# Kernel optimization log

Measured on AMD Instinct MI355X. Metric: run time of the kernel, lower is better.

## Reference

```python
import jax, jax.numpy as jnp
import numpy as np

# Model constants (from init_kwargs)
D, P, M_STEPS, H = 32, 8, 50, 128
INTERVAL, SIGMA = 1.0, 1.0
N = 32768


def setup_inputs() -> dict:
    key = jax.random.key(0)
    ks = jax.random.split(key, 7)
    return {
        "observations": jax.random.normal(ks[0], (P,), jnp.float32),
        "initial_states": jax.random.normal(ks[1], (N, D), jnp.float32),
        "initial_values": jax.random.normal(ks[2], (N,), jnp.float32),
        "noise": jax.random.normal(ks[3], (M_STEPS, N, D), jnp.float32),
        "W1": jax.random.normal(ks[4], (D + P + 2, H), jnp.float32) * 0.05,
        "b1": jnp.zeros((H,), jnp.float32),
        "W2": jax.random.normal(ks[5], (H, D), jnp.float32) * 0.05,
        "b2": jnp.zeros((D,), jnp.float32),
        "theta": jax.random.uniform(ks[6], (1,), jnp.float32, 0.1, 1.0),
        "obs_index": 3,
        "control_required": 1,
    }


def reference(observations, initial_states, initial_values, noise,
              W1, b1, W2, b2, theta, obs_index, control_required):
    dt = jnp.float32(INTERVAL / M_STEPS)
    sqrt_dt = jnp.sqrt(dt)
    times = jnp.linspace(0.0, INTERVAL, M_STEPS + 1, dtype=jnp.float32)[:M_STEPS]
    n = initial_states.shape[0]
    Yb = jnp.broadcast_to(observations, (n, P))          # (N, p)
    t_feat = jnp.full((n, 1), float(obs_index), jnp.float32)
    cr = jnp.float32(control_required)

    def z_net(s, X):
        # Z_Network: MLP over [X, Y, s, t] -> (N, d)
        feats = jnp.concatenate([X, Yb, jnp.full((n, 1), s, jnp.float32), t_feat], axis=1)
        h = jnp.tanh(feats @ W1 + b1)
        return h @ W2 + b2

    def step(carry, xs):
        X, V = carry
        noise_m, s = xs
        W = sqrt_dt * noise_m                            # Brownian increment (N, d)
        Z = z_net(s, X)                                  # (N, d)
        control = -jax.lax.stop_gradient(Z) * cr         # detach + flag
        drift_V = 0.5 * jnp.sum(jnp.square(Z), axis=1) + jnp.sum(control * Z, axis=1)
        V = V + dt * drift_V + jnp.sum(Z * W, axis=1)
        drift_X = -theta * X + SIGMA * control           # b(theta, X) = -theta * X (OU drift)
        X = X + dt * drift_X + SIGMA * W
        return (X, V), None

    (X, V), _ = jax.lax.scan(step, (initial_states, initial_values), (noise, times))
    return X, V
```

## Files before the change

kernel.cpp:

```cpp
#include <hip/hip_runtime.h>
#include <math.h>

#define NPART 32768
#define MS 50
#define BLOCK 256

typedef __attribute__((ext_vector_type(8))) short bfrag;
typedef __attribute__((ext_vector_type(4))) float ffrag;

__device__ __forceinline__ unsigned short f2bf(float x) {
    unsigned u = __float_as_uint(x);
    u += 0x7fffu + ((u >> 16) & 1u);
    return (unsigned short)(u >> 16);
}

#if __has_builtin(__builtin_amdgcn_cvt_pk_bf16_f32)
typedef __attribute__((ext_vector_type(2))) __bf16 bf16x2;
__device__ __forceinline__ unsigned pk2(float a, float b) {
    bf16x2 r = __builtin_amdgcn_cvt_pk_bf16_f32(a, b);
    return __builtin_bit_cast(unsigned, r);
}
#else
__device__ __forceinline__ unsigned pk2(float a, float b) {
    return (unsigned)f2bf(a) | ((unsigned)f2bf(b) << 16);
}
#endif

__device__ __forceinline__ float fast_tanh(float x) {
    float e = __expf(2.0f * x);
    return 1.0f - __fdividef(2.0f, e + 1.0f);
}

__global__ __launch_bounds__(BLOCK, 2)
void fused_sde_mfma(const float* __restrict__ obs,
                    const float* __restrict__ x0,
                    const float* __restrict__ v0,
                    const float* __restrict__ noise,
                    const float* __restrict__ gW1,
                    const float* __restrict__ gb1,
                    const float* __restrict__ gW2,
                    const float* __restrict__ gb2,
                    const float* __restrict__ gtheta,
                    const int* __restrict__ gobs_idx,
                    const int* __restrict__ gctrl,
                    float* __restrict__ outX,
                    float* __restrict__ outV)
{
    __shared__ __align__(16) float Zlds[4][16][36];

    const int tid  = threadIdx.x;
    const int w    = tid >> 6;
    const int lane = tid & 63;
    const int p    = lane & 15;
    const int q    = lane >> 4;
    const int part = blockIdx.x * 64 + w * 16 + p;

    const float theta = gtheta[0];
    const float tfeat = (float)gobs_idx[0];
    const float cr    = (float)gctrl[0];
    const float dt      = 1.0f / (float)MS;
    const float sqrt_dt = sqrtf(dt);
    const float ax  = 1.0f - dt * theta;
    const float bcr = dt * cr;
    const float kv  = dt * (0.5f - cr);

    bfrag A1[8];
    #pragma unroll
    for (int mt = 0; mt < 8; ++mt) {
        const int h = 16 * mt + p;
        bfrag a;
        #pragma unroll
        for (int j = 0; j < 8; ++j)
            a[j] = (short)f2bf(gW1[(8 * q + j) * 128 + h]);
        A1[mt] = a;
    }

    bfrag B2[2][4];
    #pragma unroll
    for (int nt = 0; nt < 2; ++nt) {
        #pragma unroll
        for (int kt = 0; kt < 4; ++kt) {
            bfrag b;
            #pragma unroll
            for (int j = 0; j < 8; ++j) {
                const int h = 32 * kt + 16 * (j >> 2) + 4 * q + (j & 3);
                b[j] = (short)f2bf(gW2[h * 32 + 16 * nt + p]);
            }
            B2[nt][kt] = b;
        }
    }

    ffrag Stat[8], W1s[8];
    #pragma unroll
    for (int mt = 0; mt < 8; ++mt) {
        #pragma unroll
        for (int r = 0; r < 4; ++r) {
            const int h = 16 * mt + 4 * q + r;
            float acc = gb1[h];
            #pragma unroll
            for (int j = 0; j < 8; ++j)
                acc = fmaf(obs[j], gW1[(32 + j) * 128 + h], acc);
            acc = fmaf(tfeat, gW1[41 * 128 + h], acc);
            Stat[mt][r] = acc;
            W1s[mt][r]  = gW1[40 * 128 + h];
        }
    }

    const float bz0 = gb2[p], bz1 = gb2[16 + p];
    const ffrag Z0i = ffrag{bz0, bz0, bz0, bz0};
    const ffrag Z1i = ffrag{bz1, bz1, bz1, bz1};
    const ffrag Zzero = ffrag{0.f, 0.f, 0.f, 0.f};

    float X[8];
    {
        const float4* xp = (const float4*)(x0 + (size_t)part * 32 + 8 * q);
        float4 a = xp[0], b = xp[1];
        X[0] = a.x; X[1] = a.y; X[2] = a.z; X[3] = a.w;
        X[4] = b.x; X[5] = b.y; X[6] = b.z; X[7] = b.w;
    }
    float V = v0[part];

    const float* nbase = noise + (size_t)part * 32 + 8 * q;
    float4 nc0 = ((const float4*)nbase)[0];
    float4 nc1 = ((const float4*)nbase)[1];

    float* zbase = &Zlds[w][0][0];
    const float* zrow = &Zlds[w][p][0];

    #pragma unroll 1
    for (int m = 0; m < MS; ++m) {
        const int mn = (m + 1 < MS) ? m + 1 : m;
        const float* np = nbase + (size_t)mn * ((size_t)NPART * 32);
        float4 nn0 = ((const float4*)np)[0];
        float4 nn1 = ((const float4*)np)[1];

        int4 bxw = make_int4((int)pk2(X[0], X[1]), (int)pk2(X[2], X[3]),
                             (int)pk2(X[4], X[5]), (int)pk2(X[6], X[7]));
        bfrag BX = __builtin_bit_cast(bfrag, bxw);

        const float s = (float)m * dt;

        ffrag C[8];
        #pragma unroll
        for (int mt = 0; mt < 8; ++mt) {
            ffrag c;
            #pragma unroll
            for (int r = 0; r < 4; ++r) c[r] = fmaf(s, W1s[mt][r], Stat[mt][r]);
            C[mt] = c;
        }
        #pragma unroll
        for (int mt = 0; mt < 8; ++mt)
            C[mt] = __builtin_amdgcn_mfma_f32_16x16x32_bf16(A1[mt], BX, C[mt], 0, 0, 0);

        uint2 Hpk[8];
        #pragma unroll
        for (int mt = 0; mt < 8; ++mt) {
            const unsigned u0 = pk2(fast_tanh(C[mt][0]), fast_tanh(C[mt][1]));
            const unsigned u1 = pk2(fast_tanh(C[mt][2]), fast_tanh(C[mt][3]));
            Hpk[mt] = make_uint2(u0, u1);
        }

        ffrag D0a = Z0i, D0b = Zzero, D1a = Z1i, D1b = Zzero;
        #pragma unroll
        for (int kt = 0; kt < 4; ++kt) {
            int4 aw = make_int4((int)Hpk[2 * kt].x, (int)Hpk[2 * kt].y,
                                (int)Hpk[2 * kt + 1].x, (int)Hpk[2 * kt + 1].y);
            bfrag A = __builtin_bit_cast(bfrag, aw);
            if (kt & 1) {
                D0b = __builtin_amdgcn_mfma_f32_16x16x32_bf16(A, B2[0][kt], D0b, 0, 0, 0);
                D1b = __builtin_amdgcn_mfma_f32_16x16x32_bf16(A, B2[1][kt], D1b, 0, 0, 0);
            } else {
                D0a = __builtin_amdgcn_mfma_f32_16x16x32_bf16(A, B2[0][kt], D0a, 0, 0, 0);
                D1a = __builtin_amdgcn_mfma_f32_16x16x32_bf16(A, B2[1][kt], D1a, 0, 0, 0);
            }
        }
        ffrag D0 = D0a + D0b;
        ffrag D1 = D1a + D1b;

        #pragma unroll
        for (int r = 0; r < 4; ++r) {
            float* zr = zbase + (4 * q + r) * 36;
            zr[p]      = D0[r];
            zr[16 + p] = D1[r];
        }

        __builtin_amdgcn_wave_barrier();

        float4 z0 = *(const float4*)&zrow[8 * q];
        float4 z1 = *(const float4*)&zrow[8 * q + 4];
        float Z[8] = {z0.x, z0.y, z0.z, z0.w, z1.x, z1.y, z1.z, z1.w};
        float Nn[8] = {nc0.x, nc0.y, nc0.z, nc0.w, nc1.x, nc1.y, nc1.z, nc1.w};

        float s2 = 0.0f, sn = 0.0f;
        #pragma unroll
        for (int j = 0; j < 8; ++j) {
            s2 = fmaf(Z[j], Z[j], s2);
            sn = fmaf(Z[j], Nn[j], sn);
        }
        s2 += __shfl_xor(s2, 16); s2 += __shfl_xor(s2, 32);
        sn += __shfl_xor(sn, 16); sn += __shfl_xor(sn, 32);
        V = fmaf(kv, s2, fmaf(sqrt_dt, sn, V));

        #pragma unroll
        for (int j = 0; j < 8; ++j) {
            float t = fmaf(-bcr, Z[j], sqrt_dt * Nn[j]);
            X[j] = fmaf(ax, X[j], t);
        }

        nc0 = nn0; nc1 = nn1;

        __builtin_amdgcn_wave_barrier();
    }

    float4* xout = (float4*)(outX + (size_t)part * 32 + 8 * q);
    xout[0] = make_float4(X[0], X[1], X[2], X[3]);
    xout[1] = make_float4(X[4], X[5], X[6], X[7]);
    if (q == 0) outV[part] = V;
}

extern "C" void kernel_launch(void* const* d_in, const int* in_sizes, int n_in,
                              void* d_out, int out_size, void* d_ws, size_t ws_size,
                              hipStream_t stream) {
    const float* obs   = (const float*)d_in[0];
    const float* x0    = (const float*)d_in[1];
    const float* v0    = (const float*)d_in[2];
    const float* noise = (const float*)d_in[3];
    const float* W1    = (const float*)d_in[4];
    const float* b1    = (const float*)d_in[5];
    const float* W2    = (const float*)d_in[6];
    const float* b2    = (const float*)d_in[7];
    const float* th    = (const float*)d_in[8];
    const int*   oi    = (const int*)d_in[9];
    const int*   cr    = (const int*)d_in[10];

    float* outX = (float*)d_out;
    float* outV = outX + (size_t)NPART * 32;

    dim3 grid(NPART / 64);
    fused_sde_mfma<<<grid, BLOCK, 0, stream>>>(obs, x0, v0, noise, W1, b1, W2, b2,
                                               th, oi, cr, outX, outV);
}
```

Measured before the change: 373.0 us.

## Transpose second MFMA so Z lands in per-lane layout, removing LDS round trip

Swaps the operand order of the second-layer MFMA (weights as A, hidden activations as B) and permutes the feature ordering of W1, X and noise so each lane's output accumulator holds exactly the Z elements it needs. This removes the per-step LDS write, wave barriers and LDS read used to transpose Z. In exchange, each lane's X and noise loads become two separate float4 accesses 64 bytes apart instead of one contiguous 32-byte span.

Result: slower. 407.8 us (+9.3%).

```diff
diff --git a/kernel.cpp b/kernel.cpp
--- a/kernel.cpp
+++ b/kernel.cpp
@@ -46,8 +46,6 @@
                     float* __restrict__ outX,
                     float* __restrict__ outV)
 {
-    __shared__ __align__(16) float Zlds[4][16][36];
-
     const int tid  = threadIdx.x;
     const int w    = tid >> 6;
     const int lane = tid & 63;
@@ -70,23 +68,25 @@
         const int h = 16 * mt + p;
         bfrag a;
         #pragma unroll
-        for (int j = 0; j < 8; ++j)
-            a[j] = (short)f2bf(gW1[(8 * q + j) * 128 + h]);
+        for (int j = 0; j < 8; ++j) {
+            const int f = 4 * q + (j & 3) + 16 * (j >> 2);
+            a[j] = (short)f2bf(gW1[f * 128 + h]);
+        }
         A1[mt] = a;
     }
 
-    bfrag B2[2][4];
+    bfrag A2[2][4];
     #pragma unroll
     for (int nt = 0; nt < 2; ++nt) {
         #pragma unroll
         for (int kt = 0; kt < 4; ++kt) {
-            bfrag b;
+            bfrag a;
             #pragma unroll
             for (int j = 0; j < 8; ++j) {
                 const int h = 32 * kt + 16 * (j >> 2) + 4 * q + (j & 3);
-                b[j] = (short)f2bf(gW2[h * 32 + 16 * nt + p]);
+                a[j] = (short)f2bf(gW2[h * 32 + 16 * nt + p]);
             }
-            B2[nt][kt] = b;
+            A2[nt][kt] = a;
         }
     }
 
@@ -106,33 +106,35 @@
         }
     }
 
-    const float bz0 = gb2[p], bz1 = gb2[16 + p];
-    const ffrag Z0i = ffrag{bz0, bz0, bz0, bz0};
-    const ffrag Z1i = ffrag{bz1, bz1, bz1, bz1};
+    ffrag Z0i, Z1i;
+    {
+        float4 b = *(const float4*)(gb2 + 4 * q);
+        Z0i = ffrag{b.x, b.y, b.z, b.w};
+        float4 c = *(const float4*)(gb2 + 16 + 4 * q);
+        Z1i = ffrag{c.x, c.y, c.z, c.w};
+    }
     const ffrag Zzero = ffrag{0.f, 0.f, 0.f, 0.f};
 
     float X[8];
     {
-        const float4* xp = (const float4*)(x0 + (size_t)part * 32 + 8 * q);
-        float4 a = xp[0], b = xp[1];
+        const float* xp = x0 + (size_t)part * 32;
+        float4 a = *(const float4*)(xp + 4 * q);
+        float4 b = *(const float4*)(xp + 16 + 4 * q);
         X[0] = a.x; X[1] = a.y; X[2] = a.z; X[3] = a.w;
         X[4] = b.x; X[5] = b.y; X[6] = b.z; X[7] = b.w;
     }
     float V = v0[part];
 
-    const float* nbase = noise + (size_t)part * 32 + 8 * q;
-    float4 nc0 = ((const float4*)nbase)[0];
-    float4 nc1 = ((const float4*)nbase)[1];
-
-    float* zbase = &Zlds[w][0][0];
-    const float* zrow = &Zlds[w][p][0];
+    const float* nbase = noise + (size_t)part * 32;
+    float4 nc0 = *(const float4*)(nbase + 4 * q);
+    float4 nc1 = *(const float4*)(nbase + 16 + 4 * q);
 
     #pragma unroll 1
     for (int m = 0; m < MS; ++m) {
         const int mn = (m + 1 < MS) ? m + 1 : m;
         const float* np = nbase + (size_t)mn * ((size_t)NPART * 32);
-        float4 nn0 = ((const float4*)np)[0];
-        float4 nn1 = ((const float4*)np)[1];
+        float4 nn0 = *(const float4*)(np + 4 * q);
+        float4 nn1 = *(const float4*)(np + 16 + 4 * q);
 
         int4 bxw = make_int4((int)pk2(X[0], X[1]), (int)pk2(X[2], X[3]),
                              (int)pk2(X[4], X[5]), (int)pk2(X[6], X[7]));
@@ -163,32 +165,21 @@
         ffrag D0a = Z0i, D0b = Zzero, D1a = Z1i, D1b = Zzero;
         #pragma unroll
         for (int kt = 0; kt < 4; ++kt) {
-            int4 aw = make_int4((int)Hpk[2 * kt].x, (int)Hpk[2 * kt].y,
+            int4 hw = make_int4((int)Hpk[2 * kt].x, (int)Hpk[2 * kt].y,
                                 (int)Hpk[2 * kt + 1].x, (int)Hpk[2 * kt + 1].y);
-            bfrag A = __builtin_bit_cast(bfrag, aw);
+            bfrag Hb = __builtin_bit_cast(bfrag, hw);
             if (kt & 1) {
-                D0b = __builtin_amdgcn_mfma_f32_16x16x32_bf16(A, B2[0][kt], D0b, 0, 0, 0);
-                D1b = __builtin_amdgcn_mfma_f32_16x16x32_bf16(A, B2[1][kt], D1b, 0, 0, 0);
+                D0b = __builtin_amdgcn_mfma_f32_16x16x32_bf16(A2[0][kt], Hb, D0b, 0, 0, 0);
+                D1b = __builtin_amdgcn_mfma_f32_16x16x32_bf16(A2[1][kt], Hb, D1b, 0, 0, 0);
             } else {
-                D0a = __builtin_amdgcn_mfma_f32_16x16x32_bf16(A, B2[0][kt], D0a, 0, 0, 0);
-                D1a = __builtin_amdgcn_mfma_f32_16x16x32_bf16(A, B2[1][kt], D1a, 0, 0, 0);
+                D0a = __builtin_amdgcn_mfma_f32_16x16x32_bf16(A2[0][kt], Hb, D0a, 0, 0, 0);
+                D1a = __builtin_amdgcn_mfma_f32_16x16x32_bf16(A2[1][kt], Hb, D1a, 0, 0, 0);
             }
         }
         ffrag D0 = D0a + D0b;
         ffrag D1 = D1a + D1b;
 
-        #pragma unroll
-        for (int r = 0; r < 4; ++r) {
-            float* zr = zbase + (4 * q + r) * 36;
-            zr[p]      = D0[r];
-            zr[16 + p] = D1[r];
-        }
-
-        __builtin_amdgcn_wave_barrier();
-
-        float4 z0 = *(const float4*)&zrow[8 * q];
-        float4 z1 = *(const float4*)&zrow[8 * q + 4];
-        float Z[8] = {z0.x, z0.y, z0.z, z0.w, z1.x, z1.y, z1.z, z1.w};
+        float Z[8]  = {D0[0], D0[1], D0[2], D0[3], D1[0], D1[1], D1[2], D1[3]};
         float Nn[8] = {nc0.x, nc0.y, nc0.z, nc0.w, nc1.x, nc1.y, nc1.z, nc1.w};
 
         float s2 = 0.0f, sn = 0.0f;
@@ -208,13 +199,11 @@
         }
 
         nc0 = nn0; nc1 = nn1;
-
-        __builtin_amdgcn_wave_barrier();
-    }
-
-    float4* xout = (float4*)(outX + (size_t)part * 32 + 8 * q);
-    xout[0] = make_float4(X[0], X[1], X[2], X[3]);
-    xout[1] = make_float4(X[4], X[5], X[6], X[7]);
+    }
+
+    float* xo = outX + (size_t)part * 32;
+    *(float4*)(xo + 4 * q)      = make_float4(X[0], X[1], X[2], X[3]);
+    *(float4*)(xo + 16 + 4 * q) = make_float4(X[4], X[5], X[6], X[7]);
     if (q == 0) outV[part] = V;
 }
 
```
